# Kernel tuning notes

Hardware: AMD Instinct MI355X
Metric: run time of the kernel (lower is better)

The kernel has to match this reference:

```python
import jax, jax.numpy as jnp
import numpy as np

IS_CAUSAL = True
NEG_INF = float('-inf')


def setup_inputs() -> dict:
    key = jax.random.key(0)
    kq, kk, kv = jax.random.split(key, 3)
    B, H, S, D = 4, 16, 2048, 64
    return {
        'query': jax.random.normal(kq, (B, H, S, D), dtype=jnp.float32),
        'key': jax.random.normal(kk, (B, H, S, D), dtype=jnp.float32),
        'value': jax.random.normal(kv, (B, H, S, D), dtype=jnp.float32),
    }


def reference(query, key, value):
    # Attention(Q,K,V) = softmax(QK^T / sqrt(d_k) + causal_mask) V
    d_k = query.shape[-1]
    scale = 1.0 / np.sqrt(d_k).astype(np.float32)
    # [B,H,Sq,Sk]
    scores = jnp.einsum('bhqd,bhkd->bhqk', query, key) * scale
    if IS_CAUSAL:
        sq, sk = query.shape[-2], key.shape[-2]
        causal = jnp.triu(jnp.ones((sq, sk), dtype=bool), k=1)
        scores = jnp.where(causal[None, None, :, :], NEG_INF, scores)
    weights = jax.nn.softmax(scores, axis=-1)
    # dropout p=0.0 (eval): identity
    out = jnp.einsum('bhqk,bhkd->bhqd', weights, value)
    return out
```

## Files before the change

### kernel.cpp

```cpp
#include <hip/hip_runtime.h>
#include <stdint.h>


#define SLEN 2048
#define DHEAD 64
#define NHEADS 64
#define NELEM (SLEN * DHEAD * NHEADS)
#define PADP 72

typedef short bf16x8 __attribute__((ext_vector_type(8)));
typedef float f32x4 __attribute__((ext_vector_type(4)));

__device__ __forceinline__ uint32_t pkbf(float hi, float lo) {
    uint32_t a = __builtin_bit_cast(uint32_t, lo) + 0x8000u;
    uint32_t b = __builtin_bit_cast(uint32_t, hi) + 0x8000u;
    return __builtin_amdgcn_perm(b, a, 0x07060302u);
}
__device__ __forceinline__ unsigned short f2bf(float f) {
    return (unsigned short)((__builtin_bit_cast(uint32_t, f) + 0x8000u) >> 16);
}
__device__ __forceinline__ int swz(int row, int g) {
    return row * 64 + ((g ^ (row & 7)) << 3);
}

__global__ __launch_bounds__(256)
void convert_prep(const float* __restrict__ K, const float* __restrict__ V,
                  unsigned short* __restrict__ Kb, unsigned short* __restrict__ Vtb) {
    __shared__ unsigned short Lt[64 * 264];
    const int b = blockIdx.x, t = threadIdx.x;
    if (b < 4096) {
        const int off = (b * 256 + t) * 8;
        float4 a = *(const float4*)(K + off);
        float4 c = *(const float4*)(K + off + 4);
        uint4 o;
        o.x = pkbf(a.y, a.x); o.y = pkbf(a.w, a.z);
        o.z = pkbf(c.y, c.x); o.w = pkbf(c.w, c.z);
        *(uint4*)(Kb + off) = o;
    } else {
        const int vb2 = b - 4096;
        const int head = vb2 >> 3, kblk = vb2 & 7;
        const float* Vh = V + (size_t)head * (SLEN * DHEAD) + kblk * 256 * DHEAD;
        unsigned short* Vo = Vtb + (size_t)head * (SLEN * DHEAD) + kblk * 256;
#pragma unroll
        for (int i = 0; i < 16; ++i) {
            int idx = t + 256 * i;
            int key = idx >> 4, d4 = idx & 15;
            float4 v = *(const float4*)(Vh + key * DHEAD + d4 * 4);
            Lt[(d4 * 4 + 0) * 264 + key] = f2bf(v.x);
            Lt[(d4 * 4 + 1) * 264 + key] = f2bf(v.y);
            Lt[(d4 * 4 + 2) * 264 + key] = f2bf(v.z);
            Lt[(d4 * 4 + 3) * 264 + key] = f2bf(v.w);
        }
        __syncthreads();
#pragma unroll
        for (int jj = 0; jj < 8; ++jj) {
            int idx = t + 256 * jj;
            int d = idx >> 5, k8 = idx & 31;
            *(uint4*)(Vo + (size_t)d * SLEN + k8 * 8) = *(const uint4*)(Lt + d * 264 + k8 * 8);
        }
    }
}

__global__ __launch_bounds__(256, 4)
void sdpa_mfma(const float* __restrict__ Qf, const unsigned short* __restrict__ Kb,
               const unsigned short* __restrict__ Vtb, float* __restrict__ Og) {
    const int n = blockIdx.x;
    const int j = n >> 8, c = n & 255;
    const int head = c & 63;
    const int A  = (c >> 6) + 4 * j;
    const int Bq = 31 - A;

    const size_t hb = (size_t)head * SLEN * DHEAD;
    const float* Qh = Qf + hb;
    const unsigned short* Kh  = Kb + hb;
    const unsigned short* Vth = Vtb + hb;
    float* Oh = Og + hb;

    const int tid  = threadIdx.x;
    const int w    = tid >> 6, lane = tid & 63;
    const int cl   = lane & 15, quad = lane >> 4;

    __shared__ unsigned short Kl[64 * 64];
    __shared__ unsigned short Vt[64 * 64];
    __shared__ unsigned short Pl[4 * 32 * PADP];

    const int qw = ((w < 2) ? A * 64 : Bq * 64) + (w & 1) * 32;
    unsigned short* Plw = Pl + w * 32 * PADP;

    bf16x8 qf[2][2];
#pragma unroll
    for (int m = 0; m < 2; ++m)
#pragma unroll
        for (int h = 0; h < 2; ++h) {
            const float* src = Qh + (size_t)(qw + m * 16 + cl) * DHEAD + h * 32 + quad * 8;
            float4 a = *(const float4*)src;
            float4 b = *(const float4*)(src + 4);
            uint4 u;
            u.x = pkbf(a.y, a.x); u.y = pkbf(a.w, a.z);
            u.z = pkbf(b.y, b.x); u.w = pkbf(b.w, b.z);
            qf[m][h] = __builtin_bit_cast(bf16x8, u);
        }

    f32x4 o[2][4];
#pragma unroll
    for (int m = 0; m < 2; ++m)
#pragma unroll
        for (int d = 0; d < 4; ++d) o[m][d] = (f32x4){0.f, 0.f, 0.f, 0.f};
    float ls[2] = {0.f, 0.f};
    const float SCL = 0.18033688f;

    const int p1 = tid + 256;
    const int srow0 = tid >> 3, sg0 = tid & 7;
    const int srow1 = p1 >> 3,  sg1 = p1 & 7;
    const int lo0 = swz(srow0, sg0), lo1 = swz(srow1, sg1);
    const size_t kS0 = (size_t)srow0 * DHEAD + sg0 * 8, kS1 = (size_t)srow1 * DHEAD + sg1 * 8;
    const size_t vS0 = (size_t)srow0 * SLEN + sg0 * 8,  vS1 = (size_t)srow1 * SLEN + sg1 * 8;

    const int ntiles = Bq + 1;
    uint4 kr0 = *(const uint4*)(Kh + kS0), kr1 = *(const uint4*)(Kh + kS1);
    uint4 vr0 = *(const uint4*)(Vth + vS0), vr1 = *(const uint4*)(Vth + vS1);

    for (int t = 0; t < ntiles; ++t) {
        const int k0 = t * 64;
        __syncthreads();
        *(uint4*)(Kl + lo0) = kr0; *(uint4*)(Kl + lo1) = kr1;
        *(uint4*)(Vt + lo0) = vr0; *(uint4*)(Vt + lo1) = vr1;
        __syncthreads();
        if (t + 1 < ntiles) {
            const size_t ko = (size_t)(k0 + 64) * DHEAD;
            kr0 = *(const uint4*)(Kh + kS0 + ko);
            kr1 = *(const uint4*)(Kh + kS1 + ko);
            vr0 = *(const uint4*)(Vth + vS0 + (k0 + 64));
            vr1 = *(const uint4*)(Vth + vS1 + (k0 + 64));
        }
        if (k0 > qw + 31) continue;
        const bool partial = (k0 + 63 > qw);

#pragma unroll
        for (int kk = 0; kk < 4; ++kk) {
            bf16x8 kb0 = __builtin_bit_cast(bf16x8, *(const uint4*)(Kl + swz(kk * 16 + cl, quad)));
            bf16x8 kb1 = __builtin_bit_cast(bf16x8, *(const uint4*)(Kl + swz(kk * 16 + cl, 4 + quad)));
            const int krel = kk * 16 + quad * 4;
#pragma unroll
            for (int qq = 0; qq < 2; ++qq) {
                f32x4 s = (f32x4){0.f, 0.f, 0.f, 0.f};
                s = __builtin_amdgcn_mfma_f32_16x16x32_bf16(kb0, qf[qq][0], s, 0, 0, 0);
                s = __builtin_amdgcn_mfma_f32_16x16x32_bf16(kb1, qf[qq][1], s, 0, 0, 0);
                float p0, p1v, p2, p3;
                if (partial) {
                    const int qrel = qw - k0 + qq * 16 + cl;
                    p0 = (krel + 0 <= qrel) ? __builtin_amdgcn_exp2f(s[0] * SCL) : 0.f;
                    p1v = (krel + 1 <= qrel) ? __builtin_amdgcn_exp2f(s[1] * SCL) : 0.f;
                    p2 = (krel + 2 <= qrel) ? __builtin_amdgcn_exp2f(s[2] * SCL) : 0.f;
                    p3 = (krel + 3 <= qrel) ? __builtin_amdgcn_exp2f(s[3] * SCL) : 0.f;
                } else {
                    p0 = __builtin_amdgcn_exp2f(s[0] * SCL);
                    p1v = __builtin_amdgcn_exp2f(s[1] * SCL);
                    p2 = __builtin_amdgcn_exp2f(s[2] * SCL);
                    p3 = __builtin_amdgcn_exp2f(s[3] * SCL);
                }
                ls[qq] += (p0 + p1v) + (p2 + p3);
                uint2 pw;
                pw.x = pkbf(p1v, p0);
                pw.y = pkbf(p3, p2);
                *(uint2*)(Plw + (qq * 16 + cl) * PADP + kk * 16 + quad * 4) = pw;
            }
        }

        bf16x8 pa[2][2];
#pragma unroll
        for (int m = 0; m < 2; ++m)
#pragma unroll
            for (int h = 0; h < 2; ++h)
                pa[m][h] = __builtin_bit_cast(bf16x8,
                    *(const uint4*)(Plw + (m * 16 + cl) * PADP + h * 32 + quad * 8));
#pragma unroll
        for (int dd = 0; dd < 4; ++dd) {
            bf16x8 vb0 = __builtin_bit_cast(bf16x8, *(const uint4*)(Vt + swz(dd * 16 + cl, quad)));
            bf16x8 vb1 = __builtin_bit_cast(bf16x8, *(const uint4*)(Vt + swz(dd * 16 + cl, 4 + quad)));
#pragma unroll
            for (int m = 0; m < 2; ++m) {
                o[m][dd] = __builtin_amdgcn_mfma_f32_16x16x32_bf16(pa[m][0], vb0, o[m][dd], 0, 0, 0);
                o[m][dd] = __builtin_amdgcn_mfma_f32_16x16x32_bf16(pa[m][1], vb1, o[m][dd], 0, 0, 0);
            }
        }
    }

#pragma unroll
    for (int qq = 0; qq < 2; ++qq) {
        float v = ls[qq];
        v += __shfl_xor(v, 16);
        v += __shfl_xor(v, 32);
        ls[qq] = v;
    }

#pragma unroll
    for (int m = 0; m < 2; ++m)
#pragma unroll
        for (int r = 0; r < 4; ++r) {
            const float inv = 1.0f / __shfl(ls[m], quad * 4 + r);
#pragma unroll
            for (int dd = 0; dd < 4; ++dd)
                Oh[(size_t)(qw + m * 16 + quad * 4 + r) * DHEAD + dd * 16 + cl] = o[m][dd][r] * inv;
        }
}

extern "C" void kernel_launch(void* const* d_in, const int* in_sizes, int n_in,
                              void* d_out, int out_size, void* d_ws, size_t ws_size,
                              hipStream_t stream) {
    const float* Q = (const float*)d_in[0];
    const float* K = (const float*)d_in[1];
    const float* V = (const float*)d_in[2];
    float*       O = (float*)d_out;

    unsigned short* Kbf  = (unsigned short*)d_ws;
    unsigned short* Vtbf = Kbf + NELEM;

    convert_prep<<<dim3(4096 + 512), dim3(256), 0, stream>>>(K, V, Kbf, Vtbf);
    sdpa_mfma<<<dim3(1024), dim3(256), 0, stream>>>(Q, Kbf, Vtbf, O);
}
```

Before: 196.4 us.

## Switch attention to 32x32x16 MFMA with register-resident P and double-buffered LDS

Rewrites the inner attention loop to use 32x32x16 bf16 MFMA tiles instead of 16x16x32, computing S^T so that P stays in registers. P is repacked with v_cvt_pk_bf16_f32 and v_permlane32_swap instead of a round trip through LDS. K/V shared tiles are double-buffered, which removes one __syncthreads per iteration, and s_setprio hints are added around the MFMA sections. This aims to cut LDS traffic and barrier overhead, at the cost of higher register pressure from the 16-wide accumulators and a dependence on gfx950-specific instructions.

```diff
diff --git a/kernel.cpp b/kernel.cpp
--- a/kernel.cpp
+++ b/kernel.cpp
@@ -6,10 +6,9 @@
 #define DHEAD 64
 #define NHEADS 64
 #define NELEM (SLEN * DHEAD * NHEADS)
-#define PADP 72
 
 typedef short bf16x8 __attribute__((ext_vector_type(8)));
-typedef float f32x4 __attribute__((ext_vector_type(4)));
+typedef float f32x16 __attribute__((ext_vector_type(16)));
 
 __device__ __forceinline__ uint32_t pkbf(float hi, float lo) {
     uint32_t a = __builtin_bit_cast(uint32_t, lo) + 0x8000u;
@@ -78,35 +77,28 @@
 
     const int tid  = threadIdx.x;
     const int w    = tid >> 6, lane = tid & 63;
-    const int cl   = lane & 15, quad = lane >> 4;
-
-    __shared__ unsigned short Kl[64 * 64];
-    __shared__ unsigned short Vt[64 * 64];
-    __shared__ unsigned short Pl[4 * 32 * PADP];
+    const int q32  = lane & 31, hi = lane >> 5;
+
+    __shared__ __align__(16) unsigned short Kl[2][64 * 64];
+    __shared__ __align__(16) unsigned short Vl[2][64 * 64];
 
     const int qw = ((w < 2) ? A * 64 : Bq * 64) + (w & 1) * 32;
-    unsigned short* Plw = Pl + w * 32 * PADP;
-
-    bf16x8 qf[2][2];
-#pragma unroll
-    for (int m = 0; m < 2; ++m)
-#pragma unroll
-        for (int h = 0; h < 2; ++h) {
-            const float* src = Qh + (size_t)(qw + m * 16 + cl) * DHEAD + h * 32 + quad * 8;
-            float4 a = *(const float4*)src;
-            float4 b = *(const float4*)(src + 4);
-            uint4 u;
-            u.x = pkbf(a.y, a.x); u.y = pkbf(a.w, a.z);
-            u.z = pkbf(b.y, b.x); u.w = pkbf(b.w, b.z);
-            qf[m][h] = __builtin_bit_cast(bf16x8, u);
-        }
-
-    f32x4 o[2][4];
-#pragma unroll
-    for (int m = 0; m < 2; ++m)
-#pragma unroll
-        for (int d = 0; d < 4; ++d) o[m][d] = (f32x4){0.f, 0.f, 0.f, 0.f};
-    float ls[2] = {0.f, 0.f};
+
+    bf16x8 qf[4];
+#pragma unroll
+    for (int dc = 0; dc < 4; ++dc) {
+        const float* src = Qh + (size_t)(qw + q32) * DHEAD + dc * 16 + hi * 8;
+        float4 a = *(const float4*)src;
+        float4 b = *(const float4*)(src + 4);
+        uint4 u;
+        u.x = pkbf(a.y, a.x); u.y = pkbf(a.w, a.z);
+        u.z = pkbf(b.y, b.x); u.w = pkbf(b.w, b.z);
+        qf[dc] = __builtin_bit_cast(bf16x8, u);
+    }
+
+    f32x16 o0 = (f32x16)(0.0f);
+    f32x16 o1 = (f32x16)(0.0f);
+    float ls = 0.f;
     const float SCL = 0.18033688f;
 
     const int p1 = tid + 256;
@@ -122,9 +114,10 @@
 
     for (int t = 0; t < ntiles; ++t) {
         const int k0 = t * 64;
-        __syncthreads();
-        *(uint4*)(Kl + lo0) = kr0; *(uint4*)(Kl + lo1) = kr1;
-        *(uint4*)(Vt + lo0) = vr0; *(uint4*)(Vt + lo1) = vr1;
+        unsigned short* Kc = Kl[t & 1];
+        unsigned short* Vc = Vl[t & 1];
+        *(uint4*)(Kc + lo0) = kr0; *(uint4*)(Kc + lo1) = kr1;
+        *(uint4*)(Vc + lo0) = vr0; *(uint4*)(Vc + lo1) = vr1;
         __syncthreads();
         if (t + 1 < ntiles) {
             const size_t ko = (size_t)(k0 + 64) * DHEAD;
@@ -133,76 +126,72 @@
             vr0 = *(const uint4*)(Vth + vS0 + (k0 + 64));
             vr1 = *(const uint4*)(Vth + vS1 + (k0 + 64));
         }
-        if (k0 > qw + 31) continue;
-        const bool partial = (k0 + 63 > qw);
-
-#pragma unroll
-        for (int kk = 0; kk < 4; ++kk) {
-            bf16x8 kb0 = __builtin_bit_cast(bf16x8, *(const uint4*)(Kl + swz(kk * 16 + cl, quad)));
-            bf16x8 kb1 = __builtin_bit_cast(bf16x8, *(const uint4*)(Kl + swz(kk * 16 + cl, 4 + quad)));
-            const int krel = kk * 16 + quad * 4;
-#pragma unroll
-            for (int qq = 0; qq < 2; ++qq) {
-                f32x4 s = (f32x4){0.f, 0.f, 0.f, 0.f};
-                s = __builtin_amdgcn_mfma_f32_16x16x32_bf16(kb0, qf[qq][0], s, 0, 0, 0);
-                s = __builtin_amdgcn_mfma_f32_16x16x32_bf16(kb1, qf[qq][1], s, 0, 0, 0);
-                float p0, p1v, p2, p3;
-                if (partial) {
-                    const int qrel = qw - k0 + qq * 16 + cl;
-                    p0 = (krel + 0 <= qrel) ? __builtin_amdgcn_exp2f(s[0] * SCL) : 0.f;
-                    p1v = (krel + 1 <= qrel) ? __builtin_amdgcn_exp2f(s[1] * SCL) : 0.f;
-                    p2 = (krel + 2 <= qrel) ? __builtin_amdgcn_exp2f(s[2] * SCL) : 0.f;
-                    p3 = (krel + 3 <= qrel) ? __builtin_amdgcn_exp2f(s[3] * SCL) : 0.f;
-                } else {
-                    p0 = __builtin_amdgcn_exp2f(s[0] * SCL);
-                    p1v = __builtin_amdgcn_exp2f(s[1] * SCL);
-                    p2 = __builtin_amdgcn_exp2f(s[2] * SCL);
-                    p3 = __builtin_amdgcn_exp2f(s[3] * SCL);
-                }
-                ls[qq] += (p0 + p1v) + (p2 + p3);
-                uint2 pw;
-                pw.x = pkbf(p1v, p0);
-                pw.y = pkbf(p3, p2);
-                *(uint2*)(Plw + (qq * 16 + cl) * PADP + kk * 16 + quad * 4) = pw;
+        if (k0 <= qw + 31) {
+            const bool partial = (k0 + 63 > qw);
+            const int qrel = qw + q32 - k0 - 4 * hi;
+#pragma unroll
+            for (int kc = 0; kc < 2; ++kc) {
+                f32x16 s = (f32x16)(0.0f);
+                __builtin_amdgcn_s_setprio(1);
+#pragma unroll
+                for (int dc = 0; dc < 4; ++dc) {
+                    bf16x8 kf = __builtin_bit_cast(bf16x8,
+                        *(const uint4*)(Kc + swz(kc * 32 + q32, 2 * dc + hi)));
+                    s = __builtin_amdgcn_mfma_f32_32x32x16_bf16(kf, qf[dc], s, 0, 0, 0);
+                }
+                __builtin_amdgcn_s_setprio(0);
+                float p[16];
+                const int qr = qrel - kc * 32;
+#pragma unroll
+                for (int r = 0; r < 16; ++r) {
+                    float e = __builtin_amdgcn_exp2f(s[r] * SCL);
+                    if (partial) {
+                        const int crow = (r & 3) + 8 * (r >> 2);
+                        e = (crow <= qr) ? e : 0.f;
+                    }
+                    p[r] = e;
+                }
+                ls += ((p[0] + p[1]) + (p[2] + p[3])) + ((p[4] + p[5]) + (p[6] + p[7]))
+                    + ((p[8] + p[9]) + (p[10] + p[11])) + ((p[12] + p[13]) + (p[14] + p[15]));
+                bf16x8 pf[2];
+#pragma unroll
+                for (int sub = 0; sub < 2; ++sub) {
+                    uint32_t w0, w1, w2, w3;
+                    asm("v_cvt_pk_bf16_f32 %0, %1, %2" : "=v"(w0) : "v"(p[8*sub+0]), "v"(p[8*sub+1]));
+                    asm("v_cvt_pk_bf16_f32 %0, %1, %2" : "=v"(w1) : "v"(p[8*sub+2]), "v"(p[8*sub+3]));
+                    asm("v_cvt_pk_bf16_f32 %0, %1, %2" : "=v"(w2) : "v"(p[8*sub+4]), "v"(p[8*sub+5]));
+                    asm("v_cvt_pk_bf16_f32 %0, %1, %2" : "=v"(w3) : "v"(p[8*sub+6]), "v"(p[8*sub+7]));
+                    asm("v_permlane32_swap_b32 %0, %1" : "+v"(w0), "+v"(w2));
+                    asm("v_permlane32_swap_b32 %0, %1" : "+v"(w1), "+v"(w3));
+                    uint4 u; u.x = w0; u.y = w1; u.z = w2; u.w = w3;
+                    pf[sub] = __builtin_bit_cast(bf16x8, u);
+                }
+                __builtin_amdgcn_s_setprio(1);
+#pragma unroll
+                for (int sub = 0; sub < 2; ++sub) {
+                    const int ks = kc * 2 + sub;
+                    bf16x8 vf0 = __builtin_bit_cast(bf16x8,
+                        *(const uint4*)(Vc + swz(q32,      2 * ks + hi)));
+                    bf16x8 vf1 = __builtin_bit_cast(bf16x8,
+                        *(const uint4*)(Vc + swz(32 + q32, 2 * ks + hi)));
+                    o0 = __builtin_amdgcn_mfma_f32_32x32x16_bf16(pf[sub], vf0, o0, 0, 0, 0);
+                    o1 = __builtin_amdgcn_mfma_f32_32x32x16_bf16(pf[sub], vf1, o1, 0, 0, 0);
+                }
+                __builtin_amdgcn_s_setprio(0);
             }
         }
-
-        bf16x8 pa[2][2];
-#pragma unroll
-        for (int m = 0; m < 2; ++m)
-#pragma unroll
-            for (int h = 0; h < 2; ++h)
-                pa[m][h] = __builtin_bit_cast(bf16x8,
-                    *(const uint4*)(Plw + (m * 16 + cl) * PADP + h * 32 + quad * 8));
-#pragma unroll
-        for (int dd = 0; dd < 4; ++dd) {
-            bf16x8 vb0 = __builtin_bit_cast(bf16x8, *(const uint4*)(Vt + swz(dd * 16 + cl, quad)));
-            bf16x8 vb1 = __builtin_bit_cast(bf16x8, *(const uint4*)(Vt + swz(dd * 16 + cl, 4 + quad)));
-#pragma unroll
-            for (int m = 0; m < 2; ++m) {
-                o[m][dd] = __builtin_amdgcn_mfma_f32_16x16x32_bf16(pa[m][0], vb0, o[m][dd], 0, 0, 0);
-                o[m][dd] = __builtin_amdgcn_mfma_f32_16x16x32_bf16(pa[m][1], vb1, o[m][dd], 0, 0, 0);
-            }
-        }
-    }
-
-#pragma unroll
-    for (int qq = 0; qq < 2; ++qq) {
-        float v = ls[qq];
-        v += __shfl_xor(v, 16);
-        v += __shfl_xor(v, 32);
-        ls[qq] = v;
-    }
-
-#pragma unroll
-    for (int m = 0; m < 2; ++m)
-#pragma unroll
-        for (int r = 0; r < 4; ++r) {
-            const float inv = 1.0f / __shfl(ls[m], quad * 4 + r);
-#pragma unroll
-            for (int dd = 0; dd < 4; ++dd)
-                Oh[(size_t)(qw + m * 16 + quad * 4 + r) * DHEAD + dd * 16 + cl] = o[m][dd][r] * inv;
-        }
+    }
+
+    float lst = ls + __shfl_xor(ls, 32);
+
+#pragma unroll
+    for (int r = 0; r < 16; ++r) {
+        const int crow = (r & 3) + 8 * (r >> 2) + 4 * hi;
+        const float inv = 1.0f / __shfl(lst, crow);
+        float* dst = Oh + (size_t)(qw + crow) * DHEAD + q32;
+        dst[0]  = o0[r] * inv;
+        dst[32] = o1[r] * inv;
+    }
 }
 
 extern "C" void kernel_launch(void* const* d_in, const int* in_sizes, int n_in,
```

After: 208.6 us. +6.2%, slower.

## Fuse K/V bf16 conversion and V transpose into attention kernel

Applied to the files above, without the earlier changes.

Removes the separate pre-pass kernel that converted K to bf16 and wrote a transposed bf16 V to workspace. The attention kernel now loads fp32 K and V directly, packs them to bf16 in registers and scatters V transposed into the swizzled LDS tile. This removes one launch and a full write and read of the bf16 workspace. In exchange, each block reads fp32 data, twice the bytes of bf16, and each K/V tile is reconverted by every block that uses it. The V path also adds many scalar 16-bit LDS stores per tile.

```diff
diff --git a/kernel.cpp b/kernel.cpp
--- a/kernel.cpp
+++ b/kernel.cpp
@@ -4,8 +4,6 @@
 
 #define SLEN 2048
 #define DHEAD 64
-#define NHEADS 64
-#define NELEM (SLEN * DHEAD * NHEADS)
 #define PADP 72
 
 typedef short bf16x8 __attribute__((ext_vector_type(8)));
@@ -23,47 +21,9 @@
     return row * 64 + ((g ^ (row & 7)) << 3);
 }
 
-__global__ __launch_bounds__(256)
-void convert_prep(const float* __restrict__ K, const float* __restrict__ V,
-                  unsigned short* __restrict__ Kb, unsigned short* __restrict__ Vtb) {
-    __shared__ unsigned short Lt[64 * 264];
-    const int b = blockIdx.x, t = threadIdx.x;
-    if (b < 4096) {
-        const int off = (b * 256 + t) * 8;
-        float4 a = *(const float4*)(K + off);
-        float4 c = *(const float4*)(K + off + 4);
-        uint4 o;
-        o.x = pkbf(a.y, a.x); o.y = pkbf(a.w, a.z);
-        o.z = pkbf(c.y, c.x); o.w = pkbf(c.w, c.z);
-        *(uint4*)(Kb + off) = o;
-    } else {
-        const int vb2 = b - 4096;
-        const int head = vb2 >> 3, kblk = vb2 & 7;
-        const float* Vh = V + (size_t)head * (SLEN * DHEAD) + kblk * 256 * DHEAD;
-        unsigned short* Vo = Vtb + (size_t)head * (SLEN * DHEAD) + kblk * 256;
-#pragma unroll
-        for (int i = 0; i < 16; ++i) {
-            int idx = t + 256 * i;
-            int key = idx >> 4, d4 = idx & 15;
-            float4 v = *(const float4*)(Vh + key * DHEAD + d4 * 4);
-            Lt[(d4 * 4 + 0) * 264 + key] = f2bf(v.x);
-            Lt[(d4 * 4 + 1) * 264 + key] = f2bf(v.y);
-            Lt[(d4 * 4 + 2) * 264 + key] = f2bf(v.z);
-            Lt[(d4 * 4 + 3) * 264 + key] = f2bf(v.w);
-        }
-        __syncthreads();
-#pragma unroll
-        for (int jj = 0; jj < 8; ++jj) {
-            int idx = t + 256 * jj;
-            int d = idx >> 5, k8 = idx & 31;
-            *(uint4*)(Vo + (size_t)d * SLEN + k8 * 8) = *(const uint4*)(Lt + d * 264 + k8 * 8);
-        }
-    }
-}
-
 __global__ __launch_bounds__(256, 4)
-void sdpa_mfma(const float* __restrict__ Qf, const unsigned short* __restrict__ Kb,
-               const unsigned short* __restrict__ Vtb, float* __restrict__ Og) {
+void sdpa_fused(const float* __restrict__ Qf, const float* __restrict__ Kf,
+                const float* __restrict__ Vf, float* __restrict__ Og) {
     const int n = blockIdx.x;
     const int j = n >> 8, c = n & 255;
     const int head = c & 63;
@@ -72,8 +32,8 @@
 
     const size_t hb = (size_t)head * SLEN * DHEAD;
     const float* Qh = Qf + hb;
-    const unsigned short* Kh  = Kb + hb;
-    const unsigned short* Vth = Vtb + hb;
+    const float* Kh = Kf + hb;
+    const float* Vh = Vf + hb;
     float* Oh = Og + hb;
 
     const int tid  = threadIdx.x;
@@ -109,29 +69,60 @@
     float ls[2] = {0.f, 0.f};
     const float SCL = 0.18033688f;
 
-    const int p1 = tid + 256;
     const int srow0 = tid >> 3, sg0 = tid & 7;
-    const int srow1 = p1 >> 3,  sg1 = p1 & 7;
-    const int lo0 = swz(srow0, sg0), lo1 = swz(srow1, sg1);
-    const size_t kS0 = (size_t)srow0 * DHEAD + sg0 * 8, kS1 = (size_t)srow1 * DHEAD + sg1 * 8;
-    const size_t vS0 = (size_t)srow0 * SLEN + sg0 * 8,  vS1 = (size_t)srow1 * SLEN + sg1 * 8;
+    const int srow1 = srow0 + 32;
+    const int lo0 = swz(srow0, sg0), lo1 = swz(srow1, sg0);
+    const size_t kF0 = (size_t)srow0 * DHEAD + sg0 * 8;
+    const size_t kF1 = (size_t)srow1 * DHEAD + sg0 * 8;
+
+    const int vkey = tid & 63, vdb = tid >> 6;
+    const int kg = vkey >> 3, ko = vkey & 7;
+    const int vr0w = vdb * 16;
+    const size_t vF = (size_t)vkey * DHEAD + vdb * 16;
 
     const int ntiles = Bq + 1;
-    uint4 kr0 = *(const uint4*)(Kh + kS0), kr1 = *(const uint4*)(Kh + kS1);
-    uint4 vr0 = *(const uint4*)(Vth + vS0), vr1 = *(const uint4*)(Vth + vS1);
+    float4 ka, kb_, kc_, kd_;
+    float4 va, vb_, vc_, vd_;
+    ka  = *(const float4*)(Kh + kF0);
+    kb_ = *(const float4*)(Kh + kF0 + 4);
+    kc_ = *(const float4*)(Kh + kF1);
+    kd_ = *(const float4*)(Kh + kF1 + 4);
+    va  = *(const float4*)(Vh + vF);
+    vb_ = *(const float4*)(Vh + vF + 4);
+    vc_ = *(const float4*)(Vh + vF + 8);
+    vd_ = *(const float4*)(Vh + vF + 12);
 
     for (int t = 0; t < ntiles; ++t) {
         const int k0 = t * 64;
         __syncthreads();
-        *(uint4*)(Kl + lo0) = kr0; *(uint4*)(Kl + lo1) = kr1;
-        *(uint4*)(Vt + lo0) = vr0; *(uint4*)(Vt + lo1) = vr1;
+        {
+            uint4 u;
+            u.x = pkbf(ka.y, ka.x);   u.y = pkbf(ka.w, ka.z);
+            u.z = pkbf(kb_.y, kb_.x); u.w = pkbf(kb_.w, kb_.z);
+            *(uint4*)(Kl + lo0) = u;
+            u.x = pkbf(kc_.y, kc_.x); u.y = pkbf(kc_.w, kc_.z);
+            u.z = pkbf(kd_.y, kd_.x); u.w = pkbf(kd_.w, kd_.z);
+            *(uint4*)(Kl + lo1) = u;
+        }
+        {
+#define VW(rr, val) Vt[(vr0w + (rr)) * 64 + (((kg) ^ ((rr) & 7)) << 3) + ko] = f2bf(val)
+            VW(0,  va.x);  VW(1,  va.y);  VW(2,  va.z);  VW(3,  va.w);
+            VW(4,  vb_.x); VW(5,  vb_.y); VW(6,  vb_.z); VW(7,  vb_.w);
+            VW(8,  vc_.x); VW(9,  vc_.y); VW(10, vc_.z); VW(11, vc_.w);
+            VW(12, vd_.x); VW(13, vd_.y); VW(14, vd_.z); VW(15, vd_.w);
+#undef VW
+        }
         __syncthreads();
         if (t + 1 < ntiles) {
-            const size_t ko = (size_t)(k0 + 64) * DHEAD;
-            kr0 = *(const uint4*)(Kh + kS0 + ko);
-            kr1 = *(const uint4*)(Kh + kS1 + ko);
-            vr0 = *(const uint4*)(Vth + vS0 + (k0 + 64));
-            vr1 = *(const uint4*)(Vth + vS1 + (k0 + 64));
+            const size_t adv = (size_t)(k0 + 64) * DHEAD;
+            ka  = *(const float4*)(Kh + kF0 + adv);
+            kb_ = *(const float4*)(Kh + kF0 + adv + 4);
+            kc_ = *(const float4*)(Kh + kF1 + adv);
+            kd_ = *(const float4*)(Kh + kF1 + adv + 4);
+            va  = *(const float4*)(Vh + vF + adv);
+            vb_ = *(const float4*)(Vh + vF + adv + 4);
+            vc_ = *(const float4*)(Vh + vF + adv + 8);
+            vd_ = *(const float4*)(Vh + vF + adv + 12);
         }
         if (k0 > qw + 31) continue;
         const bool partial = (k0 + 63 > qw);
@@ -212,10 +203,7 @@
     const float* K = (const float*)d_in[1];
     const float* V = (const float*)d_in[2];
     float*       O = (float*)d_out;
-
-    unsigned short* Kbf  = (unsigned short*)d_ws;
-    unsigned short* Vtbf = Kbf + NELEM;
-
-    convert_prep<<<dim3(4096 + 512), dim3(256), 0, stream>>>(K, V, Kbf, Vtbf);
-    sdpa_mfma<<<dim3(1024), dim3(256), 0, stream>>>(Q, Kbf, Vtbf, O);
-}
+    (void)d_ws; (void)ws_size;
+
+    sdpa_fused<<<dim3(1024), dim3(256), 0, stream>>>(Q, K, V, O);
+}
```

Result: slower. 318.8 us (+62.4%).
